# Optimization experiments

Measured on AMD Instinct MI355X. Metric: run time of the kernel, lower is better.

The kernel has to match this reference:

```python
import jax, jax.numpy as jnp
import numpy as np

TRIM_RATIO = 0.1
B, N, D_IN, D_H, N_OUT, D_OUT = 64, 1024, 512, 1024, 10, 1


def setup_inputs() -> dict:
    key = jax.random.key(0)
    ks = jax.random.split(key, 10)
    X = jax.random.normal(ks[0], (B, N, D_IN), dtype=jnp.float32)
    # ragged valid lengths in [N//2, N]; guarantees num_valid > 2*k for trim_ratio=0.1
    lengths = jax.random.randint(ks[1], (B,), N // 2, N + 1)
    mask = (jnp.arange(N)[None, :] < lengths[:, None]).astype(jnp.float32)
    s_in, s_h = 1.0 / np.sqrt(D_IN), 1.0 / np.sqrt(D_H)
    W1 = jax.random.uniform(ks[2], (D_IN, D_H), jnp.float32, -s_in, s_in)
    b1 = jax.random.uniform(ks[3], (D_H,), jnp.float32, -s_in, s_in)
    W2 = jax.random.uniform(ks[4], (D_H, D_H), jnp.float32, -s_h, s_h)
    b2 = jax.random.uniform(ks[5], (D_H,), jnp.float32, -s_h, s_h)
    W3 = jax.random.uniform(ks[6], (D_H, D_H), jnp.float32, -s_h, s_h)
    b3 = jax.random.uniform(ks[7], (D_H,), jnp.float32, -s_h, s_h)
    W4 = jax.random.uniform(ks[8], (D_H, N_OUT * D_OUT), jnp.float32, -s_h, s_h)
    b4 = jax.random.uniform(ks[9], (N_OUT * D_OUT,), jnp.float32, -s_h, s_h)
    return {"X": X, "mask": mask, "W1": W1, "b1": b1, "W2": W2, "b2": b2,
            "W3": W3, "b3": b3, "W4": W4, "b4": b4}


def reference(X, mask, W1, b1, W2, b2, W3, b3, W4, b4):
    # encode MLP: [B,N,D_IN] -> [B,N,D_H]
    encoded = jax.nn.relu(jnp.einsum('bni,ih->bnh', X, W1) + b1) @ W2 + b2
    masked = encoded * mask[..., None]
    num_valid = mask.sum(axis=-1).astype(jnp.int32)                 # [B]
    k = (num_valid.astype(jnp.float32) * TRIM_RATIO).astype(jnp.int32)  # floor, as int()
    # push invalid rows to +inf so valid elements occupy the first num_valid slots after sort
    padded = jnp.where(mask[..., None] > 0, masked, jnp.inf)
    sorted_v = jnp.sort(padded, axis=1)                             # per-column sort, [B,N,D_H]
    pos = jnp.arange(N)[None, :]
    keep = (pos >= k[:, None]) & (pos < (num_valid - k)[:, None])   # [B,N]
    summed = jnp.sum(jnp.where(keep[..., None], sorted_v, 0.0), axis=1)  # [B,D_H]
    denom = (num_valid - 2 * k).astype(jnp.float32)[:, None]
    aggregated = summed / denom                                     # trimmed mean
    # decode MLP
    out = jax.nn.relu(aggregated @ W3 + b3) @ W4 + b4               # [B, N_OUT*D_OUT]
    out = out.reshape(-1, N_OUT, D_OUT).squeeze(-1)                 # [B, N_OUT]
    return out
```

## Files before the change

kernel.cpp:

```cpp
#include <hip/hip_runtime.h>


typedef _Float16 half8  __attribute__((ext_vector_type(8)));
typedef _Float16 half4v __attribute__((ext_vector_type(4)));
typedef float    floatx4 __attribute__((ext_vector_type(4)));

#define GLD_LDS(g, l)                                                                     \
  __builtin_amdgcn_global_load_lds((const __attribute__((address_space(1))) void*)(g),    \
                                   (__attribute__((address_space(3))) void*)(l), 16, 0, 0)

__global__ void prep_nv(const float* __restrict__ mask, int* __restrict__ nv_arr,
                        int* __restrict__ k_arr) {
  int b = blockIdx.x, lane = threadIdx.x;
  const float4* mp = (const float4*)(mask + (b << 10));
  float s = 0.f;
#pragma unroll
  for (int i = 0; i < 4; ++i) {
    float4 v = mp[lane + i * 64];
    s += v.x + v.y + v.z + v.w;
  }
#pragma unroll
  for (int off = 32; off > 0; off >>= 1) s += __shfl_xor(s, off, 64);
  if (lane == 0) {
    int nv = (int)(s + 0.5f);
    int kk = (int)((float)nv * 0.1f);
    nv_arr[b] = nv;
    k_arr[b] = kk;
  }
}

__global__ void conv_x(const float* __restrict__ X, _Float16* __restrict__ X16) {
  int i = (blockIdx.x * 256 + threadIdx.x) * 8;
  float4 a = *(const float4*)(X + i);
  float4 c = *(const float4*)(X + i + 4);
  half8 h;
  h[0] = (_Float16)a.x; h[1] = (_Float16)a.y; h[2] = (_Float16)a.z; h[3] = (_Float16)a.w;
  h[4] = (_Float16)c.x; h[5] = (_Float16)c.y; h[6] = (_Float16)c.z; h[7] = (_Float16)c.w;
  *(half8*)(X16 + i) = h;
}

__global__ void transpose_conv(const float* __restrict__ W, _Float16* __restrict__ WT,
                               int R, int C) {
  __shared__ _Float16 tile[64][65];
  int r0 = blockIdx.x * 64, c0 = blockIdx.y * 64;
  for (int i = threadIdx.x; i < 4096; i += 256) {
    int r = i >> 6, c = i & 63;
    tile[r][c] = (_Float16)W[(size_t)(r0 + r) * C + c0 + c];
  }
  __syncthreads();
  for (int i = threadIdx.x; i < 4096; i += 256) {
    int c = i >> 6, r = i & 63;
    WT[(size_t)(c0 + c) * R + r0 + r] = tile[r][c];
  }
}

template <int KDIM, int MODE>
__global__ __launch_bounds__(256, 3) void gemm_kernel(
    const _Float16* __restrict__ Aop, const _Float16* __restrict__ Bop,
    const float* __restrict__ bias, const int* __restrict__ nv_arr,
    _Float16* __restrict__ outp) {
  __shared__ __align__(16) _Float16 ldsA[128 * 64];
  __shared__ __align__(16) _Float16 ldsB[128 * 64];
  int i0, j0;
  int bid = blockIdx.x;
  int fat = (((bid >> 6) << 3) | (bid & 7)) * 128;
  int thin = ((bid >> 3) & 7) * 128;
  if (MODE == 1) {
    i0 = thin; j0 = fat;
    if ((j0 & 1023) >= nv_arr[j0 >> 10]) return;
  } else {
    i0 = fat; j0 = thin;
    if ((i0 & 1023) >= nv_arr[i0 >> 10]) return;
  }
  const int t = threadIdx.x, lane = t & 63;
  const int wv = t >> 6, wi = wv & 1, wj = wv >> 1;
  const int lr = lane & 15, q = lane >> 4;

  floatx4 acc[4][4] = {};

  const int gch = (t & 7) ^ ((t >> 3) & 7);
  const _Float16* gA[4];
  const _Float16* gB[4];
  _Float16* lA[4];
  _Float16* lB[4];
#pragma unroll
  for (int r = 0; r < 4; ++r) {
    int row = r * 32 + (t >> 3);
    gA[r] = Aop + (size_t)(i0 + row) * KDIM + gch * 8;
    gB[r] = Bop + (size_t)(j0 + row) * KDIM + gch * 8;
    lA[r] = ldsA + (r * 256 + (t & ~63)) * 8;
    lB[r] = ldsB + (r * 256 + (t & ~63)) * 8;
  }

  int aoff[4], boff[4];
#pragma unroll
  for (int mi = 0; mi < 4; ++mi) {
    int row = wi * 64 + mi * 16 + lr;
    aoff[mi] = row * 64 + ((q ^ (row & 7)) * 8);
  }
#pragma unroll
  for (int nj = 0; nj < 4; ++nj) {
    int row = wj * 64 + nj * 16 + lr;
    boff[nj] = row * 64 + ((q ^ (row & 7)) * 8);
  }

  for (int kt = 0; kt < KDIM / 64; ++kt) {
#pragma unroll
    for (int r = 0; r < 4; ++r) GLD_LDS(gA[r], lA[r]);
#pragma unroll
    for (int r = 0; r < 4; ++r) GLD_LDS(gB[r], lB[r]);
#pragma unroll
    for (int r = 0; r < 4; ++r) { gA[r] += 64; gB[r] += 64; }
    __syncthreads();
#pragma unroll
    for (int kk = 0; kk < 2; ++kk) {
      half8 af[4], bf[4];
#pragma unroll
      for (int mi = 0; mi < 4; ++mi) af[mi] = *(const half8*)&ldsA[aoff[mi] ^ (kk * 32)];
#pragma unroll
      for (int nj = 0; nj < 4; ++nj) bf[nj] = *(const half8*)&ldsB[boff[nj] ^ (kk * 32)];
#pragma unroll
      for (int mi = 0; mi < 4; ++mi)
#pragma unroll
        for (int nj = 0; nj < 4; ++nj)
          acc[mi][nj] =
              __builtin_amdgcn_mfma_f32_16x16x32_f16(af[mi], bf[nj], acc[mi][nj], 0, 0, 0);
    }
    __syncthreads();
  }

  if (MODE == 1) {
#pragma unroll
    for (int mi = 0; mi < 4; ++mi) {
      int ih = i0 + wi * 64 + mi * 16 + q * 4;
      floatx4 bb = *(const floatx4*)&bias[ih];
#pragma unroll
      for (int nj = 0; nj < 4; ++nj) {
        int j = j0 + wj * 64 + nj * 16 + lr;
        floatx4 v = acc[mi][nj];
        half4v hv;
#pragma unroll
        for (int r = 0; r < 4; ++r) hv[r] = (_Float16)fmaxf(v[r] + bb[r], 0.f);
        *(half4v*)&outp[(size_t)j * 1024 + ih] = hv;
      }
    }
  } else {
#pragma unroll
    for (int nj = 0; nj < 4; ++nj) {
      int j = j0 + wj * 64 + nj * 16 + lr;
      float bj = bias[j];
#pragma unroll
      for (int mi = 0; mi < 4; ++mi) {
        int im = i0 + wi * 64 + mi * 16 + q * 4;
        int bb = im >> 10, n = im & 1023;
        floatx4 v = acc[mi][nj];
        half4v hv;
#pragma unroll
        for (int r = 0; r < 4; ++r) hv[r] = (_Float16)(v[r] + bj);
        *(half4v*)&outp[((size_t)bb << 20) + ((size_t)j << 10) + (size_t)n] = hv;
      }
    }
  }
}

#define NB 1024
__global__ __launch_bounds__(256) void trim_kernel(const _Float16* __restrict__ encT,
                                                   const int* __restrict__ nv_arr,
                                                   const int* __restrict__ k_arr,
                                                   float* __restrict__ agg) {
  __shared__ unsigned int cnt[4 * NB];
  int t = threadIdx.x, lane = t & 63, w = t >> 6;
  int blk = blockIdx.x;
  int batch = blk >> 8;
  int h = ((blk & 255) << 2) + w;
  unsigned int* cw = cnt + w * NB;
  uint4* cp = (uint4*)cw;
  {
    uint4 z = {0u, 0u, 0u, 0u};
#pragma unroll
    for (int i = 0; i < 4; ++i) cp[lane * 4 + (i ^ ((lane >> 1) & 3))] = z;
  }

  int nv = nv_arr[batch], kk = k_arr[batch];
  const _Float16* col = encT + ((size_t)batch << 20) + ((size_t)h << 10);
  const uint4* p = (const uint4*)col + lane * 2;
  uint4 u0 = p[0], u1 = p[1];
  unsigned vals[8] = {u0.x, u0.y, u0.z, u0.w, u1.x, u1.y, u1.z, u1.w};
  int nvalid = nv - lane * 16;

  float vv[16];
  int bn[16];
#pragma unroll
  for (int d = 0; d < 8; ++d) {
    unsigned u = vals[d];
#pragma unroll
    for (int sub = 0; sub < 2; ++sub) {
      int idx = d * 2 + sub;
      unsigned short bits = (unsigned short)(sub ? (u >> 16) : (u & 0xffffu));
      _Float16 hvv;
      __builtin_memcpy(&hvv, &bits, 2);
      float v = (float)hvv;
      if (idx < nvalid) {
        v = fminf(fmaxf(v, -8.0f), 7.999f);
        int bin = (int)((v + 8.0f) * 64.0f);
        bin = min(NB - 1, bin);
        vv[idx] = v;
        bn[idx] = bin;
        int Lb = bin >> 4, jc = (bin >> 2) & 3;
        int phys = ((Lb << 2) + (jc ^ ((Lb >> 1) & 3))) * 4 + (bin & 3);
        atomicAdd(&cw[phys], 1u);
      } else {
        vv[idx] = 0.f;
        bn[idx] = -1;
      }
    }
  }

  int c[16];
  {
    uint4 rb[4];
#pragma unroll
    for (int i = 0; i < 4; ++i) rb[i] = cp[lane * 4 + (i ^ ((lane >> 1) & 3))];
#pragma unroll
    for (int i = 0; i < 4; ++i) {
      c[4 * i] = (int)rb[i].x; c[4 * i + 1] = (int)rb[i].y;
      c[4 * i + 2] = (int)rb[i].z; c[4 * i + 3] = (int)rb[i].w;
    }
  }
  int ct = 0;
#pragma unroll
  for (int i = 0; i < 16; ++i) ct += c[i];
  int ci = ct;
#pragma unroll
  for (int off = 1; off < 64; off <<= 1) {
    int cu = __shfl_up(ci, off, 64);
    if (lane >= off) ci += cu;
  }
  int cex = ci - ct;
  int r1 = kk, r2 = nv - kk;
  int p1 = -1, p2 = -1;
  {
    int run = cex;
#pragma unroll
    for (int i = 0; i < 16; ++i) {
      int cc = c[i];
      if (run < r1 && r1 <= run + cc) p1 = ((lane * 16 + i) << 12) | run;
      if (run < r2 && r2 <= run + cc) p2 = ((lane * 16 + i) << 12) | run;
      run += cc;
    }
  }
#pragma unroll
  for (int off = 32; off > 0; off >>= 1) {
    p1 = max(p1, __shfl_xor(p1, off, 64));
    p2 = max(p2, __shfl_xor(p2, off, 64));
  }
  int b1 = p1 >> 12, cex1 = p1 & 4095;
  int b2 = p2 >> 12, cex2 = p2 & 4095;
  float s1 = 0.f, s2 = 0.f, tm = 0.f;
  int c1 = 0, c2 = 0;
#pragma unroll
  for (int i = 0; i < 16; ++i) {
    int b = bn[i];
    float v = vv[i];
    if (b == b1) { s1 += v; c1++; }
    if (b == b2) { s2 += v; c2++; }
    if (b > b1 && b < b2) tm += v;
  }
#pragma unroll
  for (int off = 32; off > 0; off >>= 1) {
    s1 += __shfl_xor(s1, off, 64);
    s2 += __shfl_xor(s2, off, 64);
    tm += __shfl_xor(tm, off, 64);
    c1 += __shfl_xor(c1, off, 64);
    c2 += __shfl_xor(c2, off, 64);
  }
  float mid;
  if (b1 == b2) {
    mid = (float)(r2 - r1) * (s1 / (float)c1);
  } else {
    mid = (float)(cex1 + c1 - r1) * (s1 / (float)c1) + tm +
          (float)(r2 - cex2) * (s2 / (float)c2);
  }
  if (lane == 0) {
    agg[(batch << 10) + h] = mid / (float)(nv - 2 * kk);
  }
}

__global__ void decode1(const float* __restrict__ agg, const float* __restrict__ W3,
                        const float* __restrict__ b3, float* __restrict__ A3) {
  __shared__ float al[1024];
  int b = blockIdx.x;
  int h = blockIdx.y * 256 + threadIdx.x;
  for (int i = threadIdx.x; i < 1024; i += 256) al[i] = agg[(b << 10) + i];
  __syncthreads();
  float acc = b3[h];
#pragma unroll 8
  for (int k2 = 0; k2 < 1024; ++k2) acc = fmaf(al[k2], W3[(size_t)k2 * 1024 + h], acc);
  A3[(b << 10) + h] = fmaxf(acc, 0.f);
}

__global__ void decode2(const float* __restrict__ A3, const float* __restrict__ W4,
                        const float* __restrict__ b4, float* __restrict__ outp) {
  __shared__ float red[4][10];
  int b = blockIdx.x, t = threadIdx.x, lane = t & 63, w = t >> 6;
  float part[10];
#pragma unroll
  for (int o = 0; o < 10; ++o) part[o] = 0.f;
#pragma unroll
  for (int jj = 0; jj < 4; ++jj) {
    int h2 = jj * 256 + t;
    float a = A3[(b << 10) + h2];
#pragma unroll
    for (int o = 0; o < 10; ++o) part[o] = fmaf(a, W4[h2 * 10 + o], part[o]);
  }
#pragma unroll
  for (int o = 0; o < 10; ++o)
#pragma unroll
    for (int off = 32; off > 0; off >>= 1) part[o] += __shfl_xor(part[o], off, 64);
  if (lane == 0)
#pragma unroll
    for (int o = 0; o < 10; ++o) red[w][o] = part[o];
  __syncthreads();
  if (t < 10) outp[b * 10 + t] = b4[t] + red[0][t] + red[1][t] + red[2][t] + red[3][t];
}

extern "C" void kernel_launch(void* const* d_in, const int* in_sizes, int n_in,
                              void* d_out, int out_size, void* d_ws, size_t ws_size,
                              hipStream_t stream) {
  const float* X = (const float*)d_in[0];
  const float* mask = (const float*)d_in[1];
  const float* W1 = (const float*)d_in[2];
  const float* b1 = (const float*)d_in[3];
  const float* W2 = (const float*)d_in[4];
  const float* b2 = (const float*)d_in[5];
  const float* W3 = (const float*)d_in[6];
  const float* b3 = (const float*)d_in[7];
  const float* W4 = (const float*)d_in[8];
  const float* b4 = (const float*)d_in[9];
  float* outp = (float*)d_out;
  char* ws = (char*)d_ws;

  _Float16* X16 = (_Float16*)(ws);
  _Float16* H1 = (_Float16*)(ws + 67108864ull);
  _Float16* encT = (_Float16*)(ws + 201326592ull);
  _Float16* W1T = (_Float16*)(ws + 335544320ull);
  _Float16* W2T = (_Float16*)(ws + 336592896ull);
  float* agg = (float*)(ws + 338690048ull);
  float* A3 = (float*)(ws + 338952192ull);
  int* nv_arr = (int*)(ws + 339214336ull);
  int* k_arr = (int*)(ws + 339214592ull);

  prep_nv<<<64, 64, 0, stream>>>(mask, nv_arr, k_arr);
  conv_x<<<16384, 256, 0, stream>>>(X, X16);
  transpose_conv<<<dim3(8, 16), 256, 0, stream>>>(W1, W1T, 512, 1024);
  transpose_conv<<<dim3(16, 16), 256, 0, stream>>>(W2, W2T, 1024, 1024);
  gemm_kernel<512, 1><<<4096, 256, 0, stream>>>(W1T, X16, b1, nv_arr, H1);
  gemm_kernel<1024, 2><<<4096, 256, 0, stream>>>(H1, W2T, b2, nv_arr, encT);
  trim_kernel<<<16384, 256, 0, stream>>>(encT, nv_arr, k_arr, agg);
  decode1<<<dim3(64, 4), 256, 0, stream>>>(agg, W3, b3, A3);
  decode2<<<64, 256, 0, stream>>>(A3, W4, b4, outp);
}
```

Baseline: 582.8 us.

## Double-buffer GEMM LDS tiles with K=32 steps to overlap loads and MFMA

The GEMM main loop now keeps two LDS buffers, each holding a K=32 slice, replacing the single K=64 buffer. The next slice's global-to-LDS loads are issued before the MFMAs on the current slice, so each iteration needs one barrier instead of two. The cost is twice as many loop iterations and barriers per K, and a 4-way instead of 8-way XOR swizzle on the narrower LDS rows, which could add bank conflicts. LDS footprint is unchanged.

```diff
diff --git a/kernel.cpp b/kernel.cpp
--- a/kernel.cpp
+++ b/kernel.cpp
@@ -59,8 +59,8 @@
     const _Float16* __restrict__ Aop, const _Float16* __restrict__ Bop,
     const float* __restrict__ bias, const int* __restrict__ nv_arr,
     _Float16* __restrict__ outp) {
-  __shared__ __align__(16) _Float16 ldsA[128 * 64];
-  __shared__ __align__(16) _Float16 ldsB[128 * 64];
+  __shared__ __align__(16) _Float16 ldsA[2][128 * 32];
+  __shared__ __align__(16) _Float16 ldsB[2][128 * 32];
   int i0, j0;
   int bid = blockIdx.x;
   int fat = (((bid >> 6) << 3) | (bid & 7)) * 128;
@@ -78,56 +78,60 @@
 
   floatx4 acc[4][4] = {};
 
-  const int gch = (t & 7) ^ ((t >> 3) & 7);
-  const _Float16* gA[4];
-  const _Float16* gB[4];
-  _Float16* lA[4];
-  _Float16* lB[4];
-#pragma unroll
-  for (int r = 0; r < 4; ++r) {
-    int row = r * 32 + (t >> 3);
-    gA[r] = Aop + (size_t)(i0 + row) * KDIM + gch * 8;
-    gB[r] = Bop + (size_t)(j0 + row) * KDIM + gch * 8;
-    lA[r] = ldsA + (r * 256 + (t & ~63)) * 8;
-    lB[r] = ldsB + (r * 256 + (t & ~63)) * 8;
-  }
+  const int idx0 = t, idx1 = 256 + t;
+  const int row0 = idx0 >> 2, row1 = idx1 >> 2;
+  const int ch0 = (idx0 & 3) ^ (row0 & 3), ch1 = (idx1 & 3) ^ (row1 & 3);
+  const _Float16* gA0 = Aop + (size_t)(i0 + row0) * KDIM + ch0 * 8;
+  const _Float16* gA1 = Aop + (size_t)(i0 + row1) * KDIM + ch1 * 8;
+  const _Float16* gB0 = Bop + (size_t)(j0 + row0) * KDIM + ch0 * 8;
+  const _Float16* gB1 = Bop + (size_t)(j0 + row1) * KDIM + ch1 * 8;
+  const int ofs0 = (idx0 & ~63) * 8, ofs1 = (idx1 & ~63) * 8;
 
   int aoff[4], boff[4];
 #pragma unroll
   for (int mi = 0; mi < 4; ++mi) {
     int row = wi * 64 + mi * 16 + lr;
-    aoff[mi] = row * 64 + ((q ^ (row & 7)) * 8);
+    aoff[mi] = row * 32 + ((q ^ (row & 3)) * 8);
   }
 #pragma unroll
   for (int nj = 0; nj < 4; ++nj) {
     int row = wj * 64 + nj * 16 + lr;
-    boff[nj] = row * 64 + ((q ^ (row & 7)) * 8);
-  }
-
-  for (int kt = 0; kt < KDIM / 64; ++kt) {
-#pragma unroll
-    for (int r = 0; r < 4; ++r) GLD_LDS(gA[r], lA[r]);
-#pragma unroll
-    for (int r = 0; r < 4; ++r) GLD_LDS(gB[r], lB[r]);
-#pragma unroll
-    for (int r = 0; r < 4; ++r) { gA[r] += 64; gB[r] += 64; }
+    boff[nj] = row * 32 + ((q ^ (row & 3)) * 8);
+  }
+
+  auto stage = [&](int b) {
+    GLD_LDS(gA0, &ldsA[b][ofs0]);
+    GLD_LDS(gA1, &ldsA[b][ofs1]);
+    GLD_LDS(gB0, &ldsB[b][ofs0]);
+    GLD_LDS(gB1, &ldsB[b][ofs1]);
+    gA0 += 32; gA1 += 32; gB0 += 32; gB1 += 32;
+  };
+  auto compute = [&](int b) {
+    half8 af[4], bf[4];
+#pragma unroll
+    for (int mi = 0; mi < 4; ++mi) af[mi] = *(const half8*)&ldsA[b][aoff[mi]];
+#pragma unroll
+    for (int nj = 0; nj < 4; ++nj) bf[nj] = *(const half8*)&ldsB[b][boff[nj]];
+#pragma unroll
+    for (int mi = 0; mi < 4; ++mi)
+#pragma unroll
+      for (int nj = 0; nj < 4; ++nj)
+        acc[mi][nj] =
+            __builtin_amdgcn_mfma_f32_16x16x32_f16(af[mi], bf[nj], acc[mi][nj], 0, 0, 0);
+  };
+
+  constexpr int KT = KDIM / 32;
+  stage(0);
+  __syncthreads();
+  int cur = 0;
+#pragma unroll 2
+  for (int kt = 0; kt < KT - 1; ++kt) {
+    stage(cur ^ 1);
+    compute(cur);
     __syncthreads();
-#pragma unroll
-    for (int kk = 0; kk < 2; ++kk) {
-      half8 af[4], bf[4];
-#pragma unroll
-      for (int mi = 0; mi < 4; ++mi) af[mi] = *(const half8*)&ldsA[aoff[mi] ^ (kk * 32)];
-#pragma unroll
-      for (int nj = 0; nj < 4; ++nj) bf[nj] = *(const half8*)&ldsB[boff[nj] ^ (kk * 32)];
-#pragma unroll
-      for (int mi = 0; mi < 4; ++mi)
-#pragma unroll
-        for (int nj = 0; nj < 4; ++nj)
-          acc[mi][nj] =
-              __builtin_amdgcn_mfma_f32_16x16x32_f16(af[mi], bf[nj], acc[mi][nj], 0, 0, 0);
-    }
-    __syncthreads();
-  }
+    cur ^= 1;
+  }
+  compute(cur);
 
   if (MODE == 1) {
 #pragma unroll
```

Measured after the change: 638.2 us. 1.1x slower.

## Fuse preprocessing kernels, skip converting padded X rows, fuse decode MLP

Applied to the files above, without the earlier changes.

Merges the X fp16 conversion and both weight transposes into a single launch, and skips converting X rows beyond each batch's valid length rounded up to 128, which later GEMM tiles never read. Also fuses the two decode kernels into one per-batch kernel that keeps the hidden activation in shared memory. The fused decode uses only 64 blocks, so it has less parallelism for the W3 pass than the earlier 256-block launch.

```diff
diff --git a/kernel.cpp b/kernel.cpp
--- a/kernel.cpp
+++ b/kernel.cpp
@@ -29,20 +29,9 @@
   }
 }
 
-__global__ void conv_x(const float* __restrict__ X, _Float16* __restrict__ X16) {
-  int i = (blockIdx.x * 256 + threadIdx.x) * 8;
-  float4 a = *(const float4*)(X + i);
-  float4 c = *(const float4*)(X + i + 4);
-  half8 h;
-  h[0] = (_Float16)a.x; h[1] = (_Float16)a.y; h[2] = (_Float16)a.z; h[3] = (_Float16)a.w;
-  h[4] = (_Float16)c.x; h[5] = (_Float16)c.y; h[6] = (_Float16)c.z; h[7] = (_Float16)c.w;
-  *(half8*)(X16 + i) = h;
-}
-
-__global__ void transpose_conv(const float* __restrict__ W, _Float16* __restrict__ WT,
-                               int R, int C) {
-  __shared__ _Float16 tile[64][65];
-  int r0 = blockIdx.x * 64, c0 = blockIdx.y * 64;
+__device__ __forceinline__ void transpose_body(const float* __restrict__ W,
+                                               _Float16* __restrict__ WT, int R, int C,
+                                               int r0, int c0, _Float16 (*tile)[65]) {
   for (int i = threadIdx.x; i < 4096; i += 256) {
     int r = i >> 6, c = i & 63;
     tile[r][c] = (_Float16)W[(size_t)(r0 + r) * C + c0 + c];
@@ -51,6 +40,34 @@
   for (int i = threadIdx.x; i < 4096; i += 256) {
     int c = i >> 6, r = i & 63;
     WT[(size_t)(c0 + c) * R + r0 + r] = tile[r][c];
+  }
+}
+
+__global__ __launch_bounds__(256) void preprocess(
+    const float* __restrict__ X, _Float16* __restrict__ X16,
+    const float* __restrict__ W1, _Float16* __restrict__ W1T,
+    const float* __restrict__ W2, _Float16* __restrict__ W2T,
+    const int* __restrict__ nv_arr) {
+  __shared__ _Float16 tile[64][65];
+  int bid = blockIdx.x;
+  if (bid < 16384) {
+    int n0 = (bid << 2) & 1023;
+    int batch = bid >> 8;
+    int nv = nv_arr[batch];
+    if (n0 >= ((nv + 127) & ~127)) return;
+    int i = (bid * 256 + threadIdx.x) * 8;
+    float4 a = *(const float4*)(X + i);
+    float4 c = *(const float4*)(X + i + 4);
+    half8 h;
+    h[0] = (_Float16)a.x; h[1] = (_Float16)a.y; h[2] = (_Float16)a.z; h[3] = (_Float16)a.w;
+    h[4] = (_Float16)c.x; h[5] = (_Float16)c.y; h[6] = (_Float16)c.z; h[7] = (_Float16)c.w;
+    *(half8*)(X16 + i) = h;
+  } else if (bid < 16384 + 128) {
+    int id = bid - 16384;
+    transpose_body(W1, W1T, 512, 1024, (id & 7) * 64, (id >> 3) * 64, tile);
+  } else {
+    int id = bid - 16512;
+    transpose_body(W2, W2T, 1024, 1024, (id & 15) * 64, (id >> 4) * 64, tile);
   }
 }
 
@@ -286,30 +303,34 @@
   }
 }
 
-__global__ void decode1(const float* __restrict__ agg, const float* __restrict__ W3,
-                        const float* __restrict__ b3, float* __restrict__ A3) {
+__global__ __launch_bounds__(256) void decode(const float* __restrict__ agg,
+                                              const float* __restrict__ W3,
+                                              const float* __restrict__ b3,
+                                              const float* __restrict__ W4,
+                                              const float* __restrict__ b4,
+                                              float* __restrict__ outp) {
   __shared__ float al[1024];
-  int b = blockIdx.x;
-  int h = blockIdx.y * 256 + threadIdx.x;
-  for (int i = threadIdx.x; i < 1024; i += 256) al[i] = agg[(b << 10) + i];
-  __syncthreads();
-  float acc = b3[h];
-#pragma unroll 8
-  for (int k2 = 0; k2 < 1024; ++k2) acc = fmaf(al[k2], W3[(size_t)k2 * 1024 + h], acc);
-  A3[(b << 10) + h] = fmaxf(acc, 0.f);
-}
-
-__global__ void decode2(const float* __restrict__ A3, const float* __restrict__ W4,
-                        const float* __restrict__ b4, float* __restrict__ outp) {
+  __shared__ float a3[1024];
   __shared__ float red[4][10];
   int b = blockIdx.x, t = threadIdx.x, lane = t & 63, w = t >> 6;
+  for (int i = t; i < 1024; i += 256) al[i] = agg[(b << 10) + i];
+  __syncthreads();
+#pragma unroll
+  for (int jj = 0; jj < 4; ++jj) {
+    int h = jj * 256 + t;
+    float acc = b3[h];
+#pragma unroll 8
+    for (int k2 = 0; k2 < 1024; ++k2) acc = fmaf(al[k2], W3[(size_t)k2 * 1024 + h], acc);
+    a3[h] = fmaxf(acc, 0.f);
+  }
+  __syncthreads();
   float part[10];
 #pragma unroll
   for (int o = 0; o < 10; ++o) part[o] = 0.f;
 #pragma unroll
   for (int jj = 0; jj < 4; ++jj) {
     int h2 = jj * 256 + t;
-    float a = A3[(b << 10) + h2];
+    float a = a3[h2];
 #pragma unroll
     for (int o = 0; o < 10; ++o) part[o] = fmaf(a, W4[h2 * 10 + o], part[o]);
   }
@@ -346,17 +367,13 @@
   _Float16* W1T = (_Float16*)(ws + 335544320ull);
   _Float16* W2T = (_Float16*)(ws + 336592896ull);
   float* agg = (float*)(ws + 338690048ull);
-  float* A3 = (float*)(ws + 338952192ull);
   int* nv_arr = (int*)(ws + 339214336ull);
   int* k_arr = (int*)(ws + 339214592ull);
 
   prep_nv<<<64, 64, 0, stream>>>(mask, nv_arr, k_arr);
-  conv_x<<<16384, 256, 0, stream>>>(X, X16);
-  transpose_conv<<<dim3(8, 16), 256, 0, stream>>>(W1, W1T, 512, 1024);
-  transpose_conv<<<dim3(16, 16), 256, 0, stream>>>(W2, W2T, 1024, 1024);
+  preprocess<<<16768, 256, 0, stream>>>(X, X16, W1, W1T, W2, W2T, nv_arr);
   gemm_kernel<512, 1><<<4096, 256, 0, stream>>>(W1T, X16, b1, nv_arr, H1);
   gemm_kernel<1024, 2><<<4096, 256, 0, stream>>>(H1, W2T, b2, nv_arr, encT);
   trim_kernel<<<16384, 256, 0, stream>>>(encT, nv_arr, k_arr, agg);
-  decode1<<<dim3(64, 4), 256, 0, stream>>>(agg, W3, b3, A3);
-  decode2<<<64, 256, 0, stream>>>(A3, W4, b4, outp);
-}
+  decode<<<64, 256, 0, stream>>>(agg, W3, b3, W4, b4, outp);
+}
```

Result: slower. 754.5 us (+29.5%).
